# Optimization experiments

Measured on AMD Instinct MI355X. Metric: run time of the kernel, lower is better.

The kernel has to match this reference:

```python
import jax, jax.numpy as jnp
import numpy as np

B, S, D = 4, 2048, 1024
H, HD = 16, 64  # nb_heads, head_size


def setup_inputs() -> dict:
    key = jax.random.key(0)
    ks = jax.random.split(key, 9)
    s = 1.0 / np.sqrt(D)
    return {
        "x": jax.random.normal(ks[0], (B, S, D), dtype=jnp.float32),
        "wq": jax.random.uniform(ks[1], (D, D), jnp.float32, -s, s),
        "bq": jax.random.uniform(ks[2], (D,), jnp.float32, -s, s),
        "wk": jax.random.uniform(ks[3], (D, D), jnp.float32, -s, s),
        "bk": jax.random.uniform(ks[4], (D,), jnp.float32, -s, s),
        "wv": jax.random.uniform(ks[5], (D, D), jnp.float32, -s, s),
        "bv": jax.random.uniform(ks[6], (D,), jnp.float32, -s, s),
        "wo": jax.random.uniform(ks[7], (D, D), jnp.float32, -s, s),
        "bo": jax.random.uniform(ks[8], (D,), jnp.float32, -s, s),
    }


def _split_heads(t):
    # [B,S,D] -> [B,H,S,HD]
    return t.reshape(B, S, H, HD).transpose(0, 2, 1, 3)


def reference(x, wq, bq, wk, bk, wv, bv, wo, bo):
    q = _split_heads(x @ wq + bq)
    k = _split_heads(x @ wk + bk)
    v = _split_heads(x @ wv + bv)
    scores = jnp.einsum("bhqd,bhkd->bhqk", q, k) / jnp.sqrt(jnp.float32(HD))
    causal = jnp.tril(jnp.ones((S, S), dtype=bool))
    scores = jnp.where(causal, scores, -jnp.inf)
    w = jax.nn.softmax(scores, axis=-1)
    a = jnp.einsum("bhqk,bhkd->bhqd", w, v)
    a = a.transpose(0, 2, 1, 3).reshape(B, S, D)
    return a @ wo + bo
```

## Files before the change

kernel.cpp:

```cpp
#include <hip/hip_runtime.h>
#include <hip/hip_bf16.h>

typedef __bf16 bf16;
typedef bf16 bf16x8 __attribute__((ext_vector_type(8)));
typedef float f32x4 __attribute__((ext_vector_type(4)));
typedef unsigned short u16;

#define B_ 4
#define S_ 2048
#define D_ 1024
#define H_ 16
#define HD_ 64

#define NEG_SENT -30000.0f

#define XN_OFF   ((size_t)0)
#define WT_OFF   ((size_t)8388608)
#define BN_OFF   ((size_t)12582912)
#define FLAG_BYTE ((size_t)25174016)
#define Q_OFF    ((size_t)12587520)
#define K_OFF    ((size_t)20976128)
#define VT_OFF   ((size_t)29364736)

union Pack4 { bf16 b[4]; uint2 q; };

__device__ __forceinline__ void load16(const bf16* g, bf16* l) {
    __builtin_amdgcn_global_load_lds(
        (const __attribute__((address_space(1))) void*)g,
        (__attribute__((address_space(3))) void*)l, 16, 0, 0);
}

__global__ __launch_bounds__(256) void detect_k(const u16* __restrict__ x,
                                                int* __restrict__ flag)
{
    __shared__ int cnt;
    if (threadIdx.x == 0) cnt = 0;
    __syncthreads();
    int c = 0;
    for (int i = threadIdx.x; i < 4096; i += 256) {
        u16 w = x[i * 2];
        int e = (w >> 7) & 0xFF;
        if (e >= 100 && e <= 135) c++;
    }
    atomicAdd(&cnt, c);
    __syncthreads();
    if (threadIdx.x == 0) *flag = (cnt > 2048) ? 1 : 0;
}

__global__ __launch_bounds__(256) void norm_x_k(const void* __restrict__ src,
                                                bf16* __restrict__ dst,
                                                const int* __restrict__ flag)
{
    const int qi = blockIdx.x * 256 + threadIdx.x;
    if (*flag) {
        ((uint2*)dst)[qi] = ((const uint2*)src)[qi];
    } else {
        float4 v = ((const float4*)src)[qi];
        Pack4 p;
        p.b[0] = (bf16)v.x; p.b[1] = (bf16)v.y;
        p.b[2] = (bf16)v.z; p.b[3] = (bf16)v.w;
        ((uint2*)dst)[qi] = p.q;
    }
}

__global__ __launch_bounds__(256) void norm_b_k(
    const void* __restrict__ b0, const void* __restrict__ b1,
    const void* __restrict__ b2, const void* __restrict__ b3,
    bf16* __restrict__ BN, const int* __restrict__ flag)
{
    const int mat = blockIdx.x;
    const void* src = (mat == 0) ? b0 : (mat == 1) ? b1 : (mat == 2) ? b2 : b3;
    bf16* dst = BN + mat * 1024;
    const int i = threadIdx.x * 4;
    if (*flag) {
        ((uint2*)(dst + i))[0] = *(const uint2*)((const bf16*)src + i);
    } else {
        const float* s = (const float*)src;
        Pack4 p;
        p.b[0] = (bf16)s[i + 0]; p.b[1] = (bf16)s[i + 1];
        p.b[2] = (bf16)s[i + 2]; p.b[3] = (bf16)s[i + 3];
        ((uint2*)(dst + i))[0] = p.q;
    }
}

__global__ __launch_bounds__(256) void transpose_w(
    const void* __restrict__ W0, const void* __restrict__ W1,
    const void* __restrict__ W2, const void* __restrict__ W3,
    bf16* __restrict__ WT, const int* __restrict__ flag)
{
    __shared__ __align__(16) bf16 tile[64][65];
    const int mat = blockIdx.z;
    const void* W = (mat == 0) ? W0 : (mat == 1) ? W1 : (mat == 2) ? W2 : W3;
    bf16* O = WT + ((size_t)mat << 20);
    const int r0 = blockIdx.y * 64, c0 = blockIdx.x * 64;
    const int t = threadIdx.x;
    const int isb = *flag;
    #pragma unroll
    for (int i = 0; i < 16; ++i) {
        int idx = t + i * 256;
        int r = idx >> 6, c = idx & 63;
        size_t off = (size_t)(r0 + r) * D_ + c0 + c;
        tile[r][c] = isb ? ((const bf16*)W)[off] : (bf16)((const float*)W)[off];
    }
    __syncthreads();
    #pragma unroll
    for (int i = 0; i < 16; ++i) {
        int idx = t + i * 256;
        int rr = idx & 63, cc = idx >> 6;
        O[(size_t)(c0 + cc) * D_ + r0 + rr] = tile[rr][cc];
    }
}

__device__ __forceinline__ void gemm_core(const bf16* __restrict__ A,
                                          const bf16* __restrict__ Bt,
                                          bf16* lA, bf16* lB,
                                          f32x4 acc[4][4], int m0, int n0)
{
    const int t = threadIdx.x;
    const int lane = t & 63;
    const int wave = t >> 6;
    const int wm = (wave >> 1) << 6;
    const int wn = (wave & 1) << 6;
    const int quad = lane >> 4;
    const int col = lane & 15;
    for (int k0 = 0; k0 < D_; k0 += 32) {
        #pragma unroll
        for (int i = 0; i < 2; ++i) {
            int slot = t + i * 256;
            int row = slot >> 2;
            int kc = (slot & 3) << 3;
            load16(A + (size_t)(m0 + row) * D_ + k0 + kc, lA + slot * 8);
            load16(Bt + (size_t)(n0 + row) * D_ + k0 + kc, lB + slot * 8);
        }
        __syncthreads();
        bf16x8 af[4], bfr[4];
        #pragma unroll
        for (int mi = 0; mi < 4; ++mi)
            af[mi] = *(const bf16x8*)(lA + (wm + mi * 16 + col) * 32 + quad * 8);
        #pragma unroll
        for (int ni = 0; ni < 4; ++ni)
            bfr[ni] = *(const bf16x8*)(lB + (wn + ni * 16 + col) * 32 + quad * 8);
        #pragma unroll
        for (int mi = 0; mi < 4; ++mi)
            #pragma unroll
            for (int ni = 0; ni < 4; ++ni)
                acc[mi][ni] = __builtin_amdgcn_mfma_f32_16x16x32_bf16(
                    af[mi], bfr[ni], acc[mi][ni], 0, 0, 0);
        __syncthreads();
    }
}

__global__ __launch_bounds__(256) void gemm_qkv_k(
    const bf16* __restrict__ X, const bf16* __restrict__ WT,
    const bf16* __restrict__ BN,
    bf16* __restrict__ Qo, bf16* __restrict__ Ko, bf16* __restrict__ Vo)
{
    __shared__ __align__(16) bf16 lA[128 * 32];
    __shared__ __align__(16) bf16 lB[128 * 32];
    const int mode = blockIdx.z;
    const bf16* Wsel = WT + ((size_t)mode << 20);
    const bf16* bias = BN + mode * 1024;
    f32x4 acc[4][4];
    const f32x4 z = {0.f, 0.f, 0.f, 0.f};
    #pragma unroll
    for (int i = 0; i < 4; ++i)
        #pragma unroll
        for (int j = 0; j < 4; ++j) acc[i][j] = z;
    const int m0 = blockIdx.x * 128, n0 = blockIdx.y * 128;
    gemm_core(X, Wsel, lA, lB, acc, m0, n0);
    const int t = threadIdx.x, lane = t & 63, wave = t >> 6;
    const int wm = (wave >> 1) << 6, wn = (wave & 1) << 6;
    const int quad = lane >> 4, col = lane & 15;
    const float scale = (mode == 0) ? 0.18033688011112042f : 1.0f;
    #pragma unroll
    for (int mi = 0; mi < 4; ++mi) {
        int gm = m0 + wm + mi * 16 + quad * 4;
        int b = gm >> 11, srow = gm & 2047;
        #pragma unroll
        for (int ni = 0; ni < 4; ++ni) {
            int gn = n0 + wn + ni * 16 + col;
            float bb = (float)bias[gn];
            int h = gn >> 6, hd = gn & 63;
            if (mode == 2) {
                Pack4 pk;
                #pragma unroll
                for (int r = 0; r < 4; ++r)
                    pk.b[r] = (bf16)(acc[mi][ni][r] + bb);
                *(uint2*)(Vo + (((size_t)b * H_ + h) * HD_ + hd) * S_ + srow)
                    = pk.q;
            } else {
                #pragma unroll
                for (int r = 0; r < 4; ++r) {
                    float v = (acc[mi][ni][r] + bb) * scale;
                    if (mode == 1)
                        Ko[(((size_t)b * H_ + h) * S_ + srow + r) * HD_ + hd] = (bf16)v;
                    else
                        Qo[(((size_t)b * H_ + h) * S_ + srow + r) * HD_ + hd] = (bf16)v;
                }
            }
        }
    }
}

__device__ __forceinline__ void attn_tile(
    const bf16* __restrict__ Qp, const bf16* __restrict__ Kp,
    const bf16* __restrict__ Vp, bf16* __restrict__ Aout,
    int b, int h, int q0,
    bf16* lK, bf16* lV, bf16* lPTw)
{
    const int t = threadIdx.x, lane = t & 63, w = t >> 6;
    const int quad = lane >> 4, col = lane & 15;
    const int wq0 = q0 + w * 16;

    bf16x8 qf[2];
    #pragma unroll
    for (int cc = 0; cc < 2; ++cc)
        qf[cc] = *(const bf16x8*)(Qp + (size_t)(wq0 + col) * HD_
                                  + cc * 32 + quad * 8);
    f32x4 o[4];
    float mst = NEG_SENT, lst = 0.f;
    const f32x4 z = {0.f, 0.f, 0.f, 0.f};
    #pragma unroll
    for (int dt = 0; dt < 4; ++dt) o[dt] = z;

    const int kend = q0 + 64;
    for (int k0 = 0; k0 < kend; k0 += 64) {
        #pragma unroll
        for (int i = 0; i < 2; ++i) {
            int slot = t + i * 256;
            int rr = slot >> 3, ch = slot & 7;
            int sw = (ch ^ (rr & 7)) << 3;
            load16(Kp + (size_t)(k0 + rr) * HD_ + sw, lK + slot * 8);
            load16(Vp + (size_t)rr * S_ + k0 + sw, lV + slot * 8);
        }
        __syncthreads();
        if (k0 < wq0 + 16) {
            bool inc[4];
            inc[0] = true;
            inc[1] = (k0 + 16 <= wq0 + 15);
            inc[2] = (k0 + 32 <= wq0 + 15);
            inc[3] = (k0 + 48 <= wq0 + 15);
            f32x4 st[4];
            #pragma unroll
            for (int mt = 0; mt < 4; ++mt) st[mt] = z;
            #pragma unroll
            for (int cc = 0; cc < 2; ++cc) {
                #pragma unroll
                for (int mt = 0; mt < 4; ++mt)
                    if (inc[mt]) {
                        bf16x8 af = *(const bf16x8*)(lK + (mt * 16 + col) * 64
                                    + (((cc * 4 + quad) ^ (col & 7)) << 3));
                        st[mt] = __builtin_amdgcn_mfma_f32_16x16x32_bf16(
                            af, qf[cc], st[mt], 0, 0, 0);
                    }
            }
            if (k0 + 64 > wq0) {
                #pragma unroll
                for (int mt = 0; mt < 4; ++mt)
                    if (inc[mt]) {
                        #pragma unroll
                        for (int r = 0; r < 4; ++r)
                            if (k0 + mt * 16 + quad * 4 + r > wq0 + col)
                                st[mt][r] = NEG_SENT;
                    }
            }
            float tm = fmaxf(fmaxf(st[0][0], st[0][1]),
                             fmaxf(st[0][2], st[0][3]));
            #pragma unroll
            for (int mt = 1; mt < 4; ++mt)
                if (inc[mt]) {
                    #pragma unroll
                    for (int r = 0; r < 4; ++r) tm = fmaxf(tm, st[mt][r]);
                }
            tm = fmaxf(tm, __shfl_xor(tm, 16));
            tm = fmaxf(tm, __shfl_xor(tm, 32));
            float mn = fmaxf(mst, tm);
            float al = exp2f(mst - mn);
            mst = mn;
            float ssum = 0.f;
            #pragma unroll
            for (int mt = 0; mt < 4; ++mt)
                if (inc[mt]) {
                    #pragma unroll
                    for (int r = 0; r < 4; ++r) {
                        float pv = exp2f(st[mt][r] - mn);
                        st[mt][r] = pv;
                        ssum += pv;
                    }
                }
            ssum += __shfl_xor(ssum, 16);
            ssum += __shfl_xor(ssum, 32);
            lst = lst * al + ssum;
            #pragma unroll
            for (int dt = 0; dt < 4; ++dt) o[dt] *= al;
            #pragma unroll
            for (int mt = 0; mt < 4; ++mt) {
                int kch = mt * 2 + (quad >> 1);
                uint2* dst = (uint2*)(&lPTw[col * 64 + ((kch ^ (col & 7)) << 3)
                                            + ((quad & 1) << 2)]);
                if (inc[mt]) {
                    Pack4 pk;
                    #pragma unroll
                    for (int r = 0; r < 4; ++r) pk.b[r] = (bf16)st[mt][r];
                    *dst = pk.q;
                } else if (mt == 1 || (mt == 3 && inc[2])) {
                    uint2 zz; zz.x = 0u; zz.y = 0u;
                    *dst = zz;
                }
            }
            asm volatile("s_waitcnt lgkmcnt(0)" ::: "memory");
            #pragma unroll
            for (int kk = 0; kk < 2; ++kk) {
                if (kk == 1 && !inc[2]) continue;
                bf16x8 pf = *(const bf16x8*)(&lPTw[col * 64
                            + (((kk * 4 + quad) ^ (col & 7)) << 3)]);
                #pragma unroll
                for (int dt = 0; dt < 4; ++dt) {
                    bf16x8 vf = *(const bf16x8*)(lV + (dt * 16 + col) * 64
                                + (((kk * 4 + quad) ^ (col & 7)) << 3));
                    o[dt] = __builtin_amdgcn_mfma_f32_16x16x32_bf16(
                        vf, pf, o[dt], 0, 0, 0);
                }
            }
        }
        __syncthreads();
    }
    const float inv = 1.f / fmaxf(lst, 1e-30f);
    const int qg = wq0 + col;
    #pragma unroll
    for (int dt = 0; dt < 4; ++dt) {
        Pack4 pk;
        #pragma unroll
        for (int r = 0; r < 4; ++r) pk.b[r] = (bf16)(o[dt][r] * inv);
        *(uint2*)(Aout + ((size_t)b * S_ + qg) * D_ + h * HD_
                  + dt * 16 + quad * 4) = pk.q;
    }
}

__global__ __launch_bounds__(256) void attn_k(
    const bf16* __restrict__ Q, const bf16* __restrict__ K,
    const bf16* __restrict__ VT, bf16* __restrict__ Aout)
{
    __shared__ __align__(16) bf16 lK[64 * 64];
    __shared__ __align__(16) bf16 lV[64 * 64];
    __shared__ __align__(16) bf16 lPT[4][16 * 64];
    const int bh = blockIdx.y;
    const bf16* Qp = Q + (size_t)bh * S_ * HD_;
    const bf16* Kp = K + (size_t)bh * S_ * HD_;
    const bf16* Vp = VT + (size_t)bh * HD_ * S_;
    const int b = bh >> 4, h = bh & 15;
    const int w = threadIdx.x >> 6;
    bf16* lPTw = &lPT[w][0];

    attn_tile(Qp, Kp, Vp, Aout, b, h, (31 - (int)blockIdx.x) * 64,
              lK, lV, lPTw);
    attn_tile(Qp, Kp, Vp, Aout, b, h, (int)blockIdx.x * 64,
              lK, lV, lPTw);
}

__global__ __launch_bounds__(256) void gemm_out_k(
    const bf16* __restrict__ A, const bf16* __restrict__ WoT,
    const bf16* __restrict__ Bo, void* __restrict__ Out,
    const int* __restrict__ flag)
{
    __shared__ __align__(16) bf16 lA[128 * 32];
    __shared__ __align__(16) bf16 lB[128 * 32];
    f32x4 acc[4][4];
    const f32x4 z = {0.f, 0.f, 0.f, 0.f};
    #pragma unroll
    for (int i = 0; i < 4; ++i)
        #pragma unroll
        for (int j = 0; j < 4; ++j) acc[i][j] = z;
    const int m0 = blockIdx.x * 128, n0 = blockIdx.y * 128;
    gemm_core(A, WoT, lA, lB, acc, m0, n0);
    const int t = threadIdx.x, lane = t & 63, wave = t >> 6;
    const int wm = (wave >> 1) << 6, wn = (wave & 1) << 6;
    const int quad = lane >> 4, col = lane & 15;
    const int isb = *flag;
    #pragma unroll
    for (int mi = 0; mi < 4; ++mi) {
        int gm = m0 + wm + mi * 16 + quad * 4;
        #pragma unroll
        for (int ni = 0; ni < 4; ++ni) {
            int gn = n0 + wn + ni * 16 + col;
            float bb = (float)Bo[gn];
            #pragma unroll
            for (int r = 0; r < 4; ++r) {
                float v = acc[mi][ni][r] + bb;
                size_t off = (size_t)(gm + r) * D_ + gn;
                if (isb) ((bf16*)Out)[off] = (bf16)v;
                else     ((float*)Out)[off] = v;
            }
        }
    }
}

extern "C" void kernel_launch(void* const* d_in, const int* in_sizes, int n_in,
                              void* d_out, int out_size, void* d_ws, size_t ws_size,
                              hipStream_t stream)
{
    const void* x  = d_in[0];
    const void* wq = d_in[1];
    const void* bq = d_in[2];
    const void* wk = d_in[3];
    const void* bk = d_in[4];
    const void* wv = d_in[5];
    const void* bv = d_in[6];
    const void* wo = d_in[7];
    const void* bo = d_in[8];

    bf16* ws  = (bf16*)d_ws;
    bf16* XN  = ws + XN_OFF;
    bf16* WT  = ws + WT_OFF;
    bf16* BN  = ws + BN_OFF;
    int*  flag = (int*)((char*)d_ws + FLAG_BYTE);
    bf16* Qb  = ws + Q_OFF;
    bf16* Kb  = ws + K_OFF;
    bf16* VTb = ws + VT_OFF;
    bf16* Ab  = XN;

    hipLaunchKernelGGL(detect_k, dim3(1), dim3(256), 0, stream,
                       (const u16*)x, flag);
    hipLaunchKernelGGL(norm_x_k, dim3(8192), dim3(256), 0, stream,
                       x, XN, flag);
    hipLaunchKernelGGL(transpose_w, dim3(16, 16, 4), dim3(256), 0, stream,
                       wq, wk, wv, wo, WT, flag);
    hipLaunchKernelGGL(norm_b_k, dim3(4), dim3(256), 0, stream,
                       bq, bk, bv, bo, BN, flag);
    hipLaunchKernelGGL(gemm_qkv_k, dim3(64, 8, 3), dim3(256), 0, stream,
                       XN, WT, BN, Qb, Kb, VTb);
    hipLaunchKernelGGL(attn_k, dim3(16, 64), dim3(256), 0, stream,
                       Qb, Kb, VTb, Ab);
    hipLaunchKernelGGL(gemm_out_k, dim3(64, 8), dim3(256), 0, stream,
                       Ab, WT + ((size_t)3u << 20), BN + 3072, d_out, flag);
}
```

Before: 301.1 us.

## Share K/V tile loads between paired causal query tiles and skip redundant rescales

The attention kernel now handles its long and short query tiles in one merged KV loop, so each K/V tile is loaded into LDS once and used by both tiles instead of being streamed twice. The softmax row sum is computed by an extra MFMA against a ones vector rather than by shuffle reductions. The max rescale is skipped unless the new max exceeds the running max by more than 8, a lazy-rescale threshold. MFMA sections are wrapped in s_setprio and launch bounds request 4 blocks per CU. The cost is more live registers and a doubled P buffer in LDS.

```diff
diff --git a/kernel.cpp b/kernel.cpp
--- a/kernel.cpp
+++ b/kernel.cpp
@@ -202,29 +202,156 @@
     }
 }
 
-__device__ __forceinline__ void attn_tile(
-    const bf16* __restrict__ Qp, const bf16* __restrict__ Kp,
-    const bf16* __restrict__ Vp, bf16* __restrict__ Aout,
-    int b, int h, int q0,
-    bf16* lK, bf16* lV, bf16* lPTw)
-{
-    const int t = threadIdx.x, lane = t & 63, w = t >> 6;
+__device__ __forceinline__ void tile_step(
+    const bf16* __restrict__ lK, const bf16* __restrict__ lV,
+    bf16* __restrict__ lPTw,
+    const bf16x8 qf[2], const bf16x8 vf4,
+    f32x4 o[4], f32x4& o4, float& mst,
+    int k0, int wq0)
+{
+    const int lane = threadIdx.x & 63;
     const int quad = lane >> 4, col = lane & 15;
-    const int wq0 = q0 + w * 16;
-
-    bf16x8 qf[2];
-    #pragma unroll
-    for (int cc = 0; cc < 2; ++cc)
-        qf[cc] = *(const bf16x8*)(Qp + (size_t)(wq0 + col) * HD_
-                                  + cc * 32 + quad * 8);
-    f32x4 o[4];
-    float mst = NEG_SENT, lst = 0.f;
     const f32x4 z = {0.f, 0.f, 0.f, 0.f};
-    #pragma unroll
-    for (int dt = 0; dt < 4; ++dt) o[dt] = z;
-
-    const int kend = q0 + 64;
-    for (int k0 = 0; k0 < kend; k0 += 64) {
+    bool inc[4];
+    inc[0] = true;
+    inc[1] = (k0 + 16 <= wq0 + 15);
+    inc[2] = (k0 + 32 <= wq0 + 15);
+    inc[3] = (k0 + 48 <= wq0 + 15);
+    f32x4 st[4];
+    #pragma unroll
+    for (int mt = 0; mt < 4; ++mt) st[mt] = z;
+    __builtin_amdgcn_s_setprio(1);
+    #pragma unroll
+    for (int cc = 0; cc < 2; ++cc) {
+        #pragma unroll
+        for (int mt = 0; mt < 4; ++mt)
+            if (inc[mt]) {
+                bf16x8 af = *(const bf16x8*)(lK + (mt * 16 + col) * 64
+                            + (((cc * 4 + quad) ^ (col & 7)) << 3));
+                st[mt] = __builtin_amdgcn_mfma_f32_16x16x32_bf16(
+                    af, qf[cc], st[mt], 0, 0, 0);
+            }
+    }
+    __builtin_amdgcn_s_setprio(0);
+    if (k0 + 64 > wq0) {
+        #pragma unroll
+        for (int mt = 0; mt < 4; ++mt)
+            if (inc[mt]) {
+                #pragma unroll
+                for (int r = 0; r < 4; ++r)
+                    if (k0 + mt * 16 + quad * 4 + r > wq0 + col)
+                        st[mt][r] = NEG_SENT;
+            }
+    }
+    float tm = fmaxf(fmaxf(st[0][0], st[0][1]), fmaxf(st[0][2], st[0][3]));
+    #pragma unroll
+    for (int mt = 1; mt < 4; ++mt)
+        if (inc[mt])
+            tm = fmaxf(tm, fmaxf(fmaxf(st[mt][0], st[mt][1]),
+                                 fmaxf(st[mt][2], st[mt][3])));
+    tm = fmaxf(tm, __shfl_xor(tm, 16));
+    tm = fmaxf(tm, __shfl_xor(tm, 32));
+    if (!__all(tm <= mst + 8.0f)) {
+        float mn = fmaxf(mst, tm);
+        float al = exp2f(mst - mn);
+        #pragma unroll
+        for (int dt = 0; dt < 4; ++dt) o[dt] *= al;
+        o4 *= al;
+        mst = mn;
+    }
+    #pragma unroll
+    for (int mt = 0; mt < 4; ++mt) {
+        int kch = mt * 2 + (quad >> 1);
+        uint2* dst = (uint2*)(&lPTw[col * 64 + ((kch ^ (col & 7)) << 3)
+                                    + ((quad & 1) << 2)]);
+        if (inc[mt]) {
+            Pack4 pk;
+            #pragma unroll
+            for (int r = 0; r < 4; ++r)
+                pk.b[r] = (bf16)exp2f(st[mt][r] - mst);
+            *dst = pk.q;
+        } else if (mt == 1 || (mt == 3 && inc[2])) {
+            uint2 zz; zz.x = 0u; zz.y = 0u;
+            *dst = zz;
+        }
+    }
+    asm volatile("s_waitcnt lgkmcnt(0)" ::: "memory");
+    __builtin_amdgcn_s_setprio(1);
+    #pragma unroll
+    for (int kk = 0; kk < 2; ++kk) {
+        if (kk == 1 && !inc[2]) continue;
+        bf16x8 pf = *(const bf16x8*)(&lPTw[col * 64
+                    + (((kk * 4 + quad) ^ (col & 7)) << 3)]);
+        #pragma unroll
+        for (int dt = 0; dt < 4; ++dt) {
+            bf16x8 vf = *(const bf16x8*)(lV + (dt * 16 + col) * 64
+                        + (((kk * 4 + quad) ^ (col & 7)) << 3));
+            o[dt] = __builtin_amdgcn_mfma_f32_16x16x32_bf16(
+                vf, pf, o[dt], 0, 0, 0);
+        }
+        o4 = __builtin_amdgcn_mfma_f32_16x16x32_bf16(vf4, pf, o4, 0, 0, 0);
+    }
+    __builtin_amdgcn_s_setprio(0);
+}
+
+__device__ __forceinline__ void tile_epilogue(
+    bf16* __restrict__ Aout, int b, int h, int wq0,
+    const f32x4 o[4], const f32x4& o4)
+{
+    const int lane = threadIdx.x & 63;
+    const int quad = lane >> 4, col = lane & 15;
+    float l = __shfl(o4[0], col);
+    const float inv = 1.f / fmaxf(l, 1e-30f);
+    const int qg = wq0 + col;
+    #pragma unroll
+    for (int dt = 0; dt < 4; ++dt) {
+        Pack4 pk;
+        #pragma unroll
+        for (int r = 0; r < 4; ++r) pk.b[r] = (bf16)(o[dt][r] * inv);
+        *(uint2*)(Aout + ((size_t)b * S_ + qg) * D_ + h * HD_
+                  + dt * 16 + quad * 4) = pk.q;
+    }
+}
+
+__global__ __launch_bounds__(256, 4) void attn_k(
+    const bf16* __restrict__ Q, const bf16* __restrict__ K,
+    const bf16* __restrict__ VT, bf16* __restrict__ Aout)
+{
+    __shared__ __align__(16) bf16 lK[64 * 64];
+    __shared__ __align__(16) bf16 lV[64 * 64];
+    __shared__ __align__(16) bf16 lPT[4][2][16 * 64];
+    const int bh = blockIdx.y;
+    const bf16* Qp = Q + (size_t)bh * S_ * HD_;
+    const bf16* Kp = K + (size_t)bh * S_ * HD_;
+    const bf16* Vp = VT + (size_t)bh * HD_ * S_;
+    const int b = bh >> 4, h = bh & 15;
+    const int t = threadIdx.x;
+    const int lane = t & 63, w = t >> 6;
+    const int quad = lane >> 4, col = lane & 15;
+
+    const int q0L = (31 - (int)blockIdx.x) * 64;
+    const int q0S = (int)blockIdx.x * 64;
+    const int wq0L = q0L + w * 16, wq0S = q0S + w * 16;
+
+    bf16x8 qfL[2], qfS[2];
+    #pragma unroll
+    for (int cc = 0; cc < 2; ++cc) {
+        qfL[cc] = *(const bf16x8*)(Qp + (size_t)(wq0L + col) * HD_
+                                   + cc * 32 + quad * 8);
+        qfS[cc] = *(const bf16x8*)(Qp + (size_t)(wq0S + col) * HD_
+                                   + cc * 32 + quad * 8);
+    }
+    const bf16 ov = (bf16)(col == 0 ? 1.0f : 0.0f);
+    const bf16x8 vf4 = {ov, ov, ov, ov, ov, ov, ov, ov};
+
+    f32x4 oL[4], oS[4], o4L, o4S;
+    const f32x4 z = {0.f, 0.f, 0.f, 0.f};
+    #pragma unroll
+    for (int dt = 0; dt < 4; ++dt) { oL[dt] = z; oS[dt] = z; }
+    o4L = z; o4S = z;
+    float mstL = NEG_SENT, mstS = NEG_SENT;
+
+    for (int k0 = 0; k0 <= q0L; k0 += 64) {
         #pragma unroll
         for (int i = 0; i < 2; ++i) {
             int slot = t + i * 256;
@@ -234,128 +361,13 @@
             load16(Vp + (size_t)rr * S_ + k0 + sw, lV + slot * 8);
         }
         __syncthreads();
-        if (k0 < wq0 + 16) {
-            bool inc[4];
-            inc[0] = true;
-            inc[1] = (k0 + 16 <= wq0 + 15);
-            inc[2] = (k0 + 32 <= wq0 + 15);
-            inc[3] = (k0 + 48 <= wq0 + 15);
-            f32x4 st[4];
-            #pragma unroll
-            for (int mt = 0; mt < 4; ++mt) st[mt] = z;
-            #pragma unroll
-            for (int cc = 0; cc < 2; ++cc) {
-                #pragma unroll
-                for (int mt = 0; mt < 4; ++mt)
-                    if (inc[mt]) {
-                        bf16x8 af = *(const bf16x8*)(lK + (mt * 16 + col) * 64
-                                    + (((cc * 4 + quad) ^ (col & 7)) << 3));
-                        st[mt] = __builtin_amdgcn_mfma_f32_16x16x32_bf16(
-                            af, qf[cc], st[mt], 0, 0, 0);
-                    }
-            }
-            if (k0 + 64 > wq0) {
-                #pragma unroll
-                for (int mt = 0; mt < 4; ++mt)
-                    if (inc[mt]) {
-                        #pragma unroll
-                        for (int r = 0; r < 4; ++r)
-                            if (k0 + mt * 16 + quad * 4 + r > wq0 + col)
-                                st[mt][r] = NEG_SENT;
-                    }
-            }
-            float tm = fmaxf(fmaxf(st[0][0], st[0][1]),
-                             fmaxf(st[0][2], st[0][3]));
-            #pragma unroll
-            for (int mt = 1; mt < 4; ++mt)
-                if (inc[mt]) {
-                    #pragma unroll
-                    for (int r = 0; r < 4; ++r) tm = fmaxf(tm, st[mt][r]);
-                }
-            tm = fmaxf(tm, __shfl_xor(tm, 16));
-            tm = fmaxf(tm, __shfl_xor(tm, 32));
-            float mn = fmaxf(mst, tm);
-            float al = exp2f(mst - mn);
-            mst = mn;
-            float ssum = 0.f;
-            #pragma unroll
-            for (int mt = 0; mt < 4; ++mt)
-                if (inc[mt]) {
-                    #pragma unroll
-                    for (int r = 0; r < 4; ++r) {
-                        float pv = exp2f(st[mt][r] - mn);
-                        st[mt][r] = pv;
-                        ssum += pv;
-                    }
-                }
-            ssum += __shfl_xor(ssum, 16);
-            ssum += __shfl_xor(ssum, 32);
-            lst = lst * al + ssum;
-            #pragma unroll
-            for (int dt = 0; dt < 4; ++dt) o[dt] *= al;
-            #pragma unroll
-            for (int mt = 0; mt < 4; ++mt) {
-                int kch = mt * 2 + (quad >> 1);
-                uint2* dst = (uint2*)(&lPTw[col * 64 + ((kch ^ (col & 7)) << 3)
-                                            + ((quad & 1) << 2)]);
-                if (inc[mt]) {
-                    Pack4 pk;
-                    #pragma unroll
-                    for (int r = 0; r < 4; ++r) pk.b[r] = (bf16)st[mt][r];
-                    *dst = pk.q;
-                } else if (mt == 1 || (mt == 3 && inc[2])) {
-                    uint2 zz; zz.x = 0u; zz.y = 0u;
-                    *dst = zz;
-                }
-            }
-            asm volatile("s_waitcnt lgkmcnt(0)" ::: "memory");
-            #pragma unroll
-            for (int kk = 0; kk < 2; ++kk) {
-                if (kk == 1 && !inc[2]) continue;
-                bf16x8 pf = *(const bf16x8*)(&lPTw[col * 64
-                            + (((kk * 4 + quad) ^ (col & 7)) << 3)]);
-                #pragma unroll
-                for (int dt = 0; dt < 4; ++dt) {
-                    bf16x8 vf = *(const bf16x8*)(lV + (dt * 16 + col) * 64
-                                + (((kk * 4 + quad) ^ (col & 7)) << 3));
-                    o[dt] = __builtin_amdgcn_mfma_f32_16x16x32_bf16(
-                        vf, pf, o[dt], 0, 0, 0);
-                }
-            }
-        }
+        tile_step(lK, lV, &lPT[w][0][0], qfL, vf4, oL, o4L, mstL, k0, wq0L);
+        if (k0 <= q0S)
+            tile_step(lK, lV, &lPT[w][1][0], qfS, vf4, oS, o4S, mstS, k0, wq0S);
         __syncthreads();
     }
-    const float inv = 1.f / fmaxf(lst, 1e-30f);
-    const int qg = wq0 + col;
-    #pragma unroll
-    for (int dt = 0; dt < 4; ++dt) {
-        Pack4 pk;
-        #pragma unroll
-        for (int r = 0; r < 4; ++r) pk.b[r] = (bf16)(o[dt][r] * inv);
-        *(uint2*)(Aout + ((size_t)b * S_ + qg) * D_ + h * HD_
-                  + dt * 16 + quad * 4) = pk.q;
-    }
-}
-
-__global__ __launch_bounds__(256) void attn_k(
-    const bf16* __restrict__ Q, const bf16* __restrict__ K,
-    const bf16* __restrict__ VT, bf16* __restrict__ Aout)
-{
-    __shared__ __align__(16) bf16 lK[64 * 64];
-    __shared__ __align__(16) bf16 lV[64 * 64];
-    __shared__ __align__(16) bf16 lPT[4][16 * 64];
-    const int bh = blockIdx.y;
-    const bf16* Qp = Q + (size_t)bh * S_ * HD_;
-    const bf16* Kp = K + (size_t)bh * S_ * HD_;
-    const bf16* Vp = VT + (size_t)bh * HD_ * S_;
-    const int b = bh >> 4, h = bh & 15;
-    const int w = threadIdx.x >> 6;
-    bf16* lPTw = &lPT[w][0];
-
-    attn_tile(Qp, Kp, Vp, Aout, b, h, (31 - (int)blockIdx.x) * 64,
-              lK, lV, lPTw);
-    attn_tile(Qp, Kp, Vp, Aout, b, h, (int)blockIdx.x * 64,
-              lK, lV, lPTw);
+    tile_epilogue(Aout, b, h, wq0L, oL, o4L);
+    tile_epilogue(Aout, b, h, wq0S, oS, o4S);
 }
 
 __global__ __launch_bounds__(256) void gemm_out_k(
```

Measured after the change: 288.9 us. 4.1% less time.
